# Kernel optimization log

Measured on AMD Instinct MI355X. Metric: run time of the kernel, lower is better.

Reference implementation:

```python
import jax, jax.numpy as jnp
import numpy as np

B, N, DIM = 4, 2048, 64  # batch, seq_len (== gate out dim), model dim (== dim_head)
H, DH = 8, 64            # heads, dim_head


def setup_inputs() -> dict:
    key = jax.random.key(0)
    ks = jax.random.split(key, 12)
    inner = H * DH
    inp = {
        'q': jax.random.normal(ks[0], (B, N, DIM), jnp.float32),
        'k': jax.random.normal(ks[1], (B, N, DIM), jnp.float32),
        'v': jax.random.normal(ks[2], (B, N, DIM), jnp.float32),
        'Wq': jax.random.normal(ks[3], (inner, DIM), jnp.float32) * 0.05,
        'Wk': jax.random.normal(ks[4], (inner, DIM), jnp.float32) * 0.05,
        'Wv': jax.random.normal(ks[5], (inner, DIM), jnp.float32) * 0.05,
        'Wo': jax.random.normal(ks[6], (DIM, inner), jnp.float32) * 0.05,
        'bo': jax.random.normal(ks[7], (DIM,), jnp.float32) * 0.05,
        'Wg': jax.random.normal(ks[8], (N, DIM), jnp.float32) * 0.05,
        's_local': jnp.float32(1.0),
        's_long': jnp.float32(1.0),
        # recurrent compressive-memory state; positive to avoid 0/0 of zero-init buffers
        'mem': jax.random.uniform(ks[9], (H, DH, DH), jnp.float32) + 0.5,
        'mem_norm': jax.random.uniform(ks[10], (H, N, 1), jnp.float32) + 0.5,
    }
    return inp


def _heads(x, W):
    # x: (B,N,DIM) @ W.T (DIM, H*DH) -> (B,H,N,DH)
    y = x @ W.T
    return y.reshape(x.shape[0], x.shape[1], H, DH).transpose(0, 2, 1, 3)


def reference(q, k, v, Wq, Wk, Wv, Wo, bo, Wg, s_local, s_long, mem, mem_norm):
    scale = DH ** -0.5
    qh, kh, vh = _heads(q, Wq), _heads(k, Wk), _heads(v, Wv)  # (B,H,N,DH)

    # local softmax attention, down-gated by (1 - sigmoid(local scalar))
    sim = jnp.einsum('bhnd,bhmd->bhnm', qh, kh) * scale
    local_attn = jax.nn.softmax(sim, axis=-1) * (1.0 - jax.nn.sigmoid(s_local))

    # query compressive memory: elu(q) @ M / (elu(q) * norm)
    eq = jax.nn.elu(qh)
    mem_q = jnp.einsum('bhnd,hde->bhne', eq, mem) / (eq * mem_norm[None])  # (B,H,N,DH)
    gated = jax.nn.sigmoid(s_long) * jnp.einsum('bhnd,md->bhnm', mem_q, Wg)  # (B,H,N,N)

    attn = local_attn + gated
    out = jnp.einsum('bhnm,bhmd->bhnd', attn, vh)
    out = out.transpose(0, 2, 1, 3).reshape(q.shape[0], q.shape[1], H * DH)
    out = out @ Wo.T + bo  # (B,N,DIM)

    # memory update (state side effect in the original forward)
    ek = jax.nn.elu(kh)
    v_term = vh - jnp.einsum('bhnd,hde->bhne', ek, mem) / (ek * mem_norm[None])
    new_mem = mem[None] + jnp.einsum('bhnd,bhne->bhde', ek, v_term)  # (B,H,DH,DH)
    new_norm = ek.sum(-1)  # (B,H,N)
    return out, new_mem, new_norm
```

## Files before the change

### kernel.cpp

```cpp
#include <hip/hip_runtime.h>
#include <math.h>


#define B_   4
#define N_   2048
#define H_   8
#define BH_  32
#define KP   72
#define SCLK 0.18033688f

typedef __bf16 bf16x8 __attribute__((ext_vector_type(8)));
typedef __bf16 bf16x4 __attribute__((ext_vector_type(4)));
typedef short  s16x4  __attribute__((ext_vector_type(4)));
typedef float  f32x4  __attribute__((ext_vector_type(4)));

__device__ __forceinline__ float eluf(float x) {
    return x > 0.0f ? x : expm1f(x);
}

__device__ __forceinline__ float fexp2(float x) {
    return __builtin_amdgcn_exp2f(x);
}

__device__ __forceinline__ f32x4 mfma16(bf16x4 a, bf16x4 b, f32x4 c) {
#if __has_builtin(__builtin_amdgcn_mfma_f32_16x16x16_bf16)
    return __builtin_amdgcn_mfma_f32_16x16x16_bf16(a, b, c, 0, 0, 0);
#else
    s16x4 ai, bi;
    __builtin_memcpy(&ai, &a, 8);
    __builtin_memcpy(&bi, &b, 8);
    return __builtin_amdgcn_mfma_f32_16x16x16bf16_1k(ai, bi, c, 0, 0, 0);
#endif
}

__global__ __launch_bounds__(256) void k_proj(
    const float* __restrict__ q, const float* __restrict__ k, const float* __restrict__ v,
    const float* __restrict__ Wq, const float* __restrict__ Wk, const float* __restrict__ Wv,
    __bf16* __restrict__ qb, float* __restrict__ kh, __bf16* __restrict__ kb,
    __bf16* __restrict__ vb, __bf16* __restrict__ vbT)
{
    const int which = blockIdx.z;
    const int h    = blockIdx.y;
    const int row0 = blockIdx.x * 64;
    const int tid  = threadIdx.x;
    const int b = row0 >> 11, nb = row0 & 2047;

    __shared__ __align__(16) float  AsT[64][68];
    __shared__ __align__(16) float  WsT[64][68];
    __shared__ __align__(16) __bf16 Cs[64 * 72];

    if (which == 2) {
        const int w = tid >> 6, lane = tid & 63;
        const int quad = lane >> 4, m = lane & 15;
        const float* ar = v + (size_t)(row0 + w * 16 + m) * 64;
        bf16x8 a0, a1;
        #pragma unroll
        for (int j = 0; j < 8; ++j) {
            a0[j] = (__bf16)ar[quad * 8 + j];
            a1[j] = (__bf16)ar[32 + quad * 8 + j];
        }
        f32x4 acc[4];
        #pragma unroll
        for (int t = 0; t < 4; ++t) {
            const float* wr = Wv + (size_t)(h * 64 + t * 16 + m) * 64;
            bf16x8 b0, b1;
            #pragma unroll
            for (int j = 0; j < 8; ++j) {
                b0[j] = (__bf16)wr[quad * 8 + j];
                b1[j] = (__bf16)wr[32 + quad * 8 + j];
            }
            f32x4 z = {0.f, 0.f, 0.f, 0.f};
            z = __builtin_amdgcn_mfma_f32_16x16x32_bf16(a0, b0, z, 0, 0, 0);
            acc[t] = __builtin_amdgcn_mfma_f32_16x16x32_bf16(a1, b1, z, 0, 0, 0);
        }
        #pragma unroll
        for (int t = 0; t < 4; ++t)
            #pragma unroll
            for (int r = 0; r < 4; ++r)
                Cs[(w * 16 + quad * 4 + r) * 72 + t * 16 + m] = (__bf16)acc[t][r];
        __syncthreads();
        const int rr = tid >> 2, csg = (tid & 3) * 16;
        bf16x8 r0 = *(const bf16x8*)&Cs[rr * 72 + csg];
        bf16x8 r1 = *(const bf16x8*)&Cs[rr * 72 + csg + 8];
        size_t gb = ((((size_t)b * H_ + h) * N_ + nb + rr) << 6) + csg;
        *(bf16x8*)&vb[gb]     = r0;
        *(bf16x8*)&vb[gb + 8] = r1;
        const int e = tid >> 2, ns = (tid & 3) * 16;
        bf16x8 t0, t1;
        #pragma unroll
        for (int j = 0; j < 8; ++j) {
            t0[j] = Cs[(ns + j) * 72 + e];
            t1[j] = Cs[(ns + 8 + j) * 72 + e];
        }
        size_t base = (((size_t)b * H_ + h) * 64 + e) * (size_t)N_ + nb + ns;
        *(bf16x8*)&vbT[base]     = t0;
        *(bf16x8*)&vbT[base + 8] = t1;
        return;
    }

    const float* __restrict__ src = (which == 0) ? q : k;
    const float* __restrict__ W   = (which == 0) ? Wq : Wk;
    for (int s = 0; s < 16; ++s) {
        int flat = s * 256 + tid;
        int r = flat >> 6, d = flat & 63;
        AsT[d][r] = src[(size_t)(row0 + r) * 64 + d];
        WsT[d][r] = W[(size_t)(h * 64 + r) * 64 + d];
    }
    __syncthreads();

    const int ty = tid >> 4, tx = tid & 15;
    float acc[4][4];
    #pragma unroll
    for (int i = 0; i < 4; ++i)
        #pragma unroll
        for (int j = 0; j < 4; ++j) acc[i][j] = 0.0f;
    for (int kd = 0; kd < 64; ++kd) {
        float4 a4 = *(const float4*)&AsT[kd][ty * 4];
        float4 w4 = *(const float4*)&WsT[kd][tx * 4];
        float a[4] = {a4.x, a4.y, a4.z, a4.w};
        float w[4] = {w4.x, w4.y, w4.z, w4.w};
        #pragma unroll
        for (int i = 0; i < 4; ++i)
            #pragma unroll
            for (int j = 0; j < 4; ++j) acc[i][j] = fmaf(a[i], w[j], acc[i][j]);
    }

    if (which == 0) {
        #pragma unroll
        for (int i = 0; i < 4; ++i) {
            size_t idx = ((((size_t)b * H_ + h) * N_ + nb + ty * 4 + i) << 6) + tx * 4;
            bf16x4 o4 = {(__bf16)acc[i][0], (__bf16)acc[i][1],
                         (__bf16)acc[i][2], (__bf16)acc[i][3]};
            *(bf16x4*)&qb[idx] = o4;
        }
    } else {
        #pragma unroll
        for (int i = 0; i < 4; ++i) {
            size_t idx = ((((size_t)b * H_ + h) * N_ + nb + ty * 4 + i) << 6) + tx * 4;
            *(float4*)&kh[idx] = make_float4(acc[i][0], acc[i][1], acc[i][2], acc[i][3]);
            bf16x4 o4 = {(__bf16)(acc[i][0] * SCLK), (__bf16)(acc[i][1] * SCLK),
                         (__bf16)(acc[i][2] * SCLK), (__bf16)(acc[i][3] * SCLK)};
            *(bf16x4*)&kb[idx] = o4;
        }
    }
}

__global__ __launch_bounds__(256) void k_memacc(
    const float* __restrict__ kh, const __bf16* __restrict__ vb,
    const float* __restrict__ mem, const float* __restrict__ mem_norm,
    float* __restrict__ pmem, float* __restrict__ out_norm)
{
    const int chunk = blockIdx.x;
    const int bh    = blockIdx.y;
    const int h     = bh & 7;
    const int n0    = chunk * 128;

    __shared__ __align__(16) __bf16 memT_hi[64 * KP], memT_lo[64 * KP];
    __shared__ __align__(16) __bf16 ekn_hi[64 * KP],  ekn_lo[64 * KP];
    __shared__ __align__(16) __bf16 ekT_hi[64 * KP],  ekT_lo[64 * KP];
    __shared__ __align__(16) __bf16 vtT_hi[64 * KP],  vtT_lo[64 * KP];

    const int tid  = threadIdx.x;
    const int w    = tid >> 6, lane = tid & 63;
    const int quad = lane >> 4, m = lane & 15;

    for (int s = 0; s < 16; ++s) {
        int flat = s * 256 + tid;
        int d = flat >> 6, e = flat & 63;
        float mv = mem[(size_t)h * 4096 + flat];
        __bf16 hi = (__bf16)mv;
        memT_hi[e * KP + d] = hi;
        memT_lo[e * KP + d] = (__bf16)(mv - (float)hi);
    }

    bf16x8 onesv;
    #pragma unroll
    for (int j = 0; j < 8; ++j) onesv[j] = (m == 0) ? (__bf16)1.0f : (__bf16)0.0f;

    f32x4 accM[4];
    #pragma unroll
    for (int t = 0; t < 4; ++t) { f32x4 z = {0.f, 0.f, 0.f, 0.f}; accM[t] = z; }
    __syncthreads();

    for (int sub = 0; sub < 2; ++sub) {
        const int nb = n0 + sub * 64;
        for (int rr = w; rr < 64; rr += 4) {
            const int n = nb + rr;
            float ekv = eluf(kh[((size_t)bh * N_ + n) * 64 + lane]);
            __bf16 hi = (__bf16)ekv;
            __bf16 lo = (__bf16)(ekv - (float)hi);
            ekn_hi[rr * KP + lane] = hi;
            ekn_lo[rr * KP + lane] = lo;
            ekT_hi[lane * KP + rr] = hi;
            ekT_lo[lane * KP + rr] = lo;
        }
        __syncthreads();

        f32x4 km[4];
        #pragma unroll
        for (int t = 0; t < 4; ++t) { f32x4 z = {0.f, 0.f, 0.f, 0.f}; km[t] = z; }
        f32x4 nsum = {0.f, 0.f, 0.f, 0.f};
        #pragma unroll
        for (int c2 = 0; c2 < 2; ++c2) {
            bf16x8 Ah = *(const bf16x8*)&ekn_hi[(w * 16 + m) * KP + c2 * 32 + quad * 8];
            bf16x8 Al = *(const bf16x8*)&ekn_lo[(w * 16 + m) * KP + c2 * 32 + quad * 8];
            nsum = __builtin_amdgcn_mfma_f32_16x16x32_bf16(Ah, onesv, nsum, 0, 0, 0);
            nsum = __builtin_amdgcn_mfma_f32_16x16x32_bf16(Al, onesv, nsum, 0, 0, 0);
            #pragma unroll
            for (int et = 0; et < 4; ++et) {
                bf16x8 Bh = *(const bf16x8*)&memT_hi[(et * 16 + m) * KP + c2 * 32 + quad * 8];
                bf16x8 Bl = *(const bf16x8*)&memT_lo[(et * 16 + m) * KP + c2 * 32 + quad * 8];
                km[et] = __builtin_amdgcn_mfma_f32_16x16x32_bf16(Al, Bh, km[et], 0, 0, 0);
                km[et] = __builtin_amdgcn_mfma_f32_16x16x32_bf16(Ah, Bl, km[et], 0, 0, 0);
                km[et] = __builtin_amdgcn_mfma_f32_16x16x32_bf16(Ah, Bh, km[et], 0, 0, 0);
            }
        }
        if (m == 0) {
            #pragma unroll
            for (int r = 0; r < 4; ++r)
                out_norm[(size_t)bh * N_ + nb + w * 16 + quad * 4 + r] = nsum[r];
        }
        float nrmv[4];
        #pragma unroll
        for (int r = 0; r < 4; ++r)
            nrmv[r] = mem_norm[(size_t)h * N_ + nb + w * 16 + quad * 4 + r];
        #pragma unroll
        for (int et = 0; et < 4; ++et) {
            #pragma unroll
            for (int r = 0; r < 4; ++r) {
                const int nl = w * 16 + quad * 4 + r;
                const int e  = et * 16 + m;
                float vh  = (float)vb[((size_t)bh * N_ + nb + nl) * 64 + e];
                float ekv = (float)ekn_hi[nl * KP + e] + (float)ekn_lo[nl * KP + e];
                float vt  = vh - km[et][r] * __builtin_amdgcn_rcpf(ekv * nrmv[r]);
                __bf16 hi = (__bf16)vt;
                vtT_hi[e * KP + nl] = hi;
                vtT_lo[e * KP + nl] = (__bf16)(vt - (float)hi);
            }
        }
        __syncthreads();

        #pragma unroll
        for (int c2 = 0; c2 < 2; ++c2) {
            bf16x8 Ah = *(const bf16x8*)&ekT_hi[(w * 16 + m) * KP + c2 * 32 + quad * 8];
            bf16x8 Al = *(const bf16x8*)&ekT_lo[(w * 16 + m) * KP + c2 * 32 + quad * 8];
            #pragma unroll
            for (int et = 0; et < 4; ++et) {
                bf16x8 Bh = *(const bf16x8*)&vtT_hi[(et * 16 + m) * KP + c2 * 32 + quad * 8];
                bf16x8 Bl = *(const bf16x8*)&vtT_lo[(et * 16 + m) * KP + c2 * 32 + quad * 8];
                accM[et] = __builtin_amdgcn_mfma_f32_16x16x32_bf16(Al, Bh, accM[et], 0, 0, 0);
                accM[et] = __builtin_amdgcn_mfma_f32_16x16x32_bf16(Ah, Bl, accM[et], 0, 0, 0);
                accM[et] = __builtin_amdgcn_mfma_f32_16x16x32_bf16(Ah, Bh, accM[et], 0, 0, 0);
            }
        }
        __syncthreads();
    }

    const size_t base = ((size_t)chunk * BH_ + bh) * 4096;
    #pragma unroll
    for (int et = 0; et < 4; ++et)
        #pragma unroll
        for (int r = 0; r < 4; ++r)
            pmem[base + (size_t)(w * 16 + quad * 4 + r) * 64 + et * 16 + m] =
                accM[et][r];
}

__global__ __launch_bounds__(256) void k_gv(
    const float* __restrict__ Wg, const __bf16* __restrict__ vbT,
    float* __restrict__ pGv)
{
    const int chunk = blockIdx.x;
    const int bh    = blockIdx.y;
    const int n0    = chunk * 128;
    __shared__ __align__(16) __bf16 WgT[64 * 136];
    const int tid  = threadIdx.x;
    const int w    = tid >> 6, lane = tid & 63;
    const int quad = lane >> 4, m = tid & 15;

    for (int s = 0; s < 8; ++s) {
        int f4 = s * 256 + tid;
        int n = f4 >> 4, dg = (f4 & 15) * 4;
        float4 wv = *(const float4*)&Wg[(size_t)(n0 + n) * 64 + dg];
        WgT[(dg + 0) * 136 + n] = (__bf16)wv.x;
        WgT[(dg + 1) * 136 + n] = (__bf16)wv.y;
        WgT[(dg + 2) * 136 + n] = (__bf16)wv.z;
        WgT[(dg + 3) * 136 + n] = (__bf16)wv.w;
    }
    __syncthreads();

    f32x4 acc[4];
    #pragma unroll
    for (int t = 0; t < 4; ++t) { f32x4 z = {0.f, 0.f, 0.f, 0.f}; acc[t] = z; }
    #pragma unroll
    for (int c = 0; c < 4; ++c) {
        bf16x8 Af = *(const bf16x8*)&WgT[(w * 16 + m) * 136 + c * 32 + quad * 8];
        #pragma unroll
        for (int et = 0; et < 4; ++et) {
            bf16x8 Bf = *(const bf16x8*)&vbT[((size_t)bh * 64 + et * 16 + m) * N_ +
                                             n0 + c * 32 + quad * 8];
            acc[et] = __builtin_amdgcn_mfma_f32_16x16x32_bf16(Af, Bf, acc[et], 0, 0, 0);
        }
    }
    const size_t base = ((size_t)chunk * BH_ + bh) * 4096;
    #pragma unroll
    for (int et = 0; et < 4; ++et)
        #pragma unroll
        for (int r = 0; r < 4; ++r)
            pGv[base + (size_t)(w * 16 + quad * 4 + r) * 64 + et * 16 + m] =
                acc[et][r];
}

__global__ __launch_bounds__(256) void k_reduce(
    const float* __restrict__ mem, const float* __restrict__ pmem,
    const float* __restrict__ pGv, float* __restrict__ out_mem, float* __restrict__ Gv)
{
    const int idx = blockIdx.x * 256 + threadIdx.x;
    const int bh = idx >> 12, h = bh & 7, de = idx & 4095;
    float sm = mem[(size_t)h * 4096 + de];
    float sg = 0.0f;
    #pragma unroll
    for (int c = 0; c < 16; ++c) {
        sm += pmem[(size_t)c * 131072 + idx];
        sg += pGv[(size_t)c * 131072 + idx];
    }
    out_mem[idx] = sm;
    Gv[idx] = sg;
}

__global__ __launch_bounds__(256, 4) void k_flash(
    const __bf16* __restrict__ qb, const __bf16* __restrict__ kb,
    const __bf16* __restrict__ vbT, const float* __restrict__ mem,
    const float* __restrict__ mem_norm, const float* __restrict__ Gv,
    const float* __restrict__ s_local_p, const float* __restrict__ s_long_p,
    __bf16* __restrict__ o)
{
    const int n0 = blockIdx.x * 128;
    const int bh = blockIdx.y;
    const int h  = bh & 7;
    const __bf16* __restrict__ kbp = kb  + (size_t)bh * N_ * 64;
    const __bf16* __restrict__ vtp = vbT + (size_t)bh * 64 * N_;

    __shared__ __align__(16) __bf16 Kb[64 * KP];
    __shared__ __align__(16) __bf16 VT[64 * KP];
    __shared__ __align__(16) __bf16 Pw[128 * KP];
    __shared__ float lsl[128];
    __shared__ float nrm_l[128];

    const int tid  = threadIdx.x;
    const int w    = tid >> 6, lane = tid & 63;
    const int quad = lane >> 4, m = lane & 15;
    const float gl   = 1.0f - 1.0f / (1.0f + __expf(-s_local_p[0]));
    const float sigg = 1.0f / (1.0f + __expf(-s_long_p[0]));

    if (tid < 128) nrm_l[tid] = mem_norm[(size_t)h * N_ + n0 + tid];

    const size_t q0 = ((size_t)bh * N_ + n0 + w * 32 + m) * 64;
    const size_t q1 = q0 + 16 * 64;
    bf16x8 qa00 = *(const bf16x8*)&qb[q0 + quad * 8];
    bf16x8 qa01 = *(const bf16x8*)&qb[q0 + 32 + quad * 8];
    bf16x8 qa10 = *(const bf16x8*)&qb[q1 + quad * 8];
    bf16x8 qa11 = *(const bf16x8*)&qb[q1 + 32 + quad * 8];

    f32x4 O0[4], O1[4];
    #pragma unroll
    for (int t = 0; t < 4; ++t) {
        f32x4 z = {0.f, 0.f, 0.f, 0.f};
        O0[t] = z; O1[t] = z;
    }
    float lsum0 = 0.f, lsum1 = 0.f;
    const int pr0 = w * 32, pr1 = w * 32 + 16;

    const int srow = tid >> 2, scg = (tid & 3) * 16;
    bf16x8 pk0 = *(const bf16x8*)&kbp[(size_t)srow * 64 + scg];
    bf16x8 pk1 = *(const bf16x8*)&kbp[(size_t)srow * 64 + scg + 8];
    bf16x8 pv0 = *(const bf16x8*)&vtp[(size_t)srow * N_ + scg];
    bf16x8 pv1 = *(const bf16x8*)&vtp[(size_t)srow * N_ + scg + 8];

    for (int c = 0; c < 32; ++c) {
        __syncthreads();
        *(bf16x8*)&Kb[srow * KP + scg]     = pk0;
        *(bf16x8*)&Kb[srow * KP + scg + 8] = pk1;
        *(bf16x8*)&VT[srow * KP + scg]     = pv0;
        *(bf16x8*)&VT[srow * KP + scg + 8] = pv1;
        __syncthreads();
        if (c + 1 < 32) {
            const size_t kn = (size_t)((c + 1) * 64 + srow) * 64 + scg;
            const size_t vn = (size_t)srow * N_ + (c + 1) * 64 + scg;
            pk0 = *(const bf16x8*)&kbp[kn];
            pk1 = *(const bf16x8*)&kbp[kn + 8];
            pv0 = *(const bf16x8*)&vtp[vn];
            pv1 = *(const bf16x8*)&vtp[vn + 8];
        }

        f32x4 s0[4], s1[4];
        #pragma unroll
        for (int t = 0; t < 4; ++t) {
            bf16x8 ka0 = *(const bf16x8*)&Kb[(t * 16 + m) * KP + quad * 8];
            bf16x8 ka1 = *(const bf16x8*)&Kb[(t * 16 + m) * KP + 32 + quad * 8];
            f32x4 z = {0.f, 0.f, 0.f, 0.f};
            z = __builtin_amdgcn_mfma_f32_16x16x32_bf16(ka0, qa00, z, 0, 0, 0);
            s0[t] = __builtin_amdgcn_mfma_f32_16x16x32_bf16(ka1, qa01, z, 0, 0, 0);
            f32x4 z2 = {0.f, 0.f, 0.f, 0.f};
            z2 = __builtin_amdgcn_mfma_f32_16x16x32_bf16(ka0, qa10, z2, 0, 0, 0);
            s1[t] = __builtin_amdgcn_mfma_f32_16x16x32_bf16(ka1, qa11, z2, 0, 0, 0);
        }

        bf16x4 pa0[4], pa1[4];
        #pragma unroll
        for (int t = 0; t < 4; ++t) {
            float p0 = fexp2(s0[t][0]), p1 = fexp2(s0[t][1]);
            float p2 = fexp2(s0[t][2]), p3 = fexp2(s0[t][3]);
            lsum0 += p0 + p1 + p2 + p3;
            bf16x4 pk = {(__bf16)p0, (__bf16)p1, (__bf16)p2, (__bf16)p3};
            pa0[t] = pk;
            float r0 = fexp2(s1[t][0]), r1 = fexp2(s1[t][1]);
            float r2 = fexp2(s1[t][2]), r3 = fexp2(s1[t][3]);
            lsum1 += r0 + r1 + r2 + r3;
            bf16x4 rk = {(__bf16)r0, (__bf16)r1, (__bf16)r2, (__bf16)r3};
            pa1[t] = rk;
        }

        #pragma unroll
        for (int t = 0; t < 4; ++t) {
            #pragma unroll
            for (int et = 0; et < 4; ++et) {
                bf16x4 vb4 = *(const bf16x4*)&VT[(et * 16 + m) * KP + t * 16 + quad * 4];
                O0[et] = mfma16(pa0[t], vb4, O0[et]);
                O1[et] = mfma16(pa1[t], vb4, O1[et]);
            }
        }
    }

    lsum0 += __shfl_xor(lsum0, 16, 64); lsum0 += __shfl_xor(lsum0, 32, 64);
    lsum1 += __shfl_xor(lsum1, 16, 64); lsum1 += __shfl_xor(lsum1, 32, 64);
    if (lane < 16) { lsl[pr0 + lane] = lsum0; lsl[pr1 + lane] = lsum1; }

    __syncthreads();
    for (int s2 = 0; s2 < 16; ++s2) {
        int flat = s2 * 256 + tid;
        int d = flat >> 6, e = flat & 63;
        Kb[e * KP + d] = (__bf16)mem[(size_t)h * 4096 + flat];
        VT[e * KP + d] = (__bf16)Gv[(size_t)bh * 4096 + flat];
    }
    __syncthreads();

    __bf16* op = o + ((size_t)bh * N_ + n0) * 64;
    #pragma unroll
    for (int s = 0; s < 2; ++s) {
        const int prs = w * 32 + s * 16;
        bf16x8 ea0, ea1;
        #pragma unroll
        for (int j = 0; j < 8; ++j) {
            ea0[j] = (__bf16)eluf((float)(s == 0 ? qa00[j] : qa10[j]));
            ea1[j] = (__bf16)eluf((float)(s == 0 ? qa01[j] : qa11[j]));
        }
        f32x4 num[4];
        #pragma unroll
        for (int t = 0; t < 4; ++t) {
            bf16x8 b0 = *(const bf16x8*)&Kb[(t * 16 + m) * KP + quad * 8];
            bf16x8 b1 = *(const bf16x8*)&Kb[(t * 16 + m) * KP + 32 + quad * 8];
            f32x4 z = {0.f, 0.f, 0.f, 0.f};
            z = __builtin_amdgcn_mfma_f32_16x16x32_bf16(ea0, b0, z, 0, 0, 0);
            num[t] = __builtin_amdgcn_mfma_f32_16x16x32_bf16(ea1, b1, z, 0, 0, 0);
        }
        *(bf16x8*)&Pw[(prs + m) * KP + quad * 8]      = ea0;
        *(bf16x8*)&Pw[(prs + m) * KP + 32 + quad * 8] = ea1;
        asm volatile("s_waitcnt lgkmcnt(0)" ::: "memory");
        float mq[4][4];
        #pragma unroll
        for (int t = 0; t < 4; ++t)
            #pragma unroll
            for (int r = 0; r < 4; ++r) {
                float eqv = (float)Pw[(prs + quad * 4 + r) * KP + t * 16 + m];
                mq[t][r] = num[t][r] / (eqv * nrm_l[prs + quad * 4 + r]);
            }
        #pragma unroll
        for (int t = 0; t < 4; ++t)
            #pragma unroll
            for (int r = 0; r < 4; ++r)
                Pw[(prs + quad * 4 + r) * KP + t * 16 + m] = (__bf16)mq[t][r];
        asm volatile("s_waitcnt lgkmcnt(0)" ::: "memory");
        bf16x8 ma0 = *(const bf16x8*)&Pw[(prs + m) * KP + quad * 8];
        bf16x8 ma1 = *(const bf16x8*)&Pw[(prs + m) * KP + 32 + quad * 8];

        #pragma unroll
        for (int t = 0; t < 4; ++t) {
            bf16x8 g0 = *(const bf16x8*)&VT[(t * 16 + m) * KP + quad * 8];
            bf16x8 g1 = *(const bf16x8*)&VT[(t * 16 + m) * KP + 32 + quad * 8];
            f32x4 z = {0.f, 0.f, 0.f, 0.f};
            z = __builtin_amdgcn_mfma_f32_16x16x32_bf16(ma0, g0, z, 0, 0, 0);
            f32x4 o2 = __builtin_amdgcn_mfma_f32_16x16x32_bf16(ma1, g1, z, 0, 0, 0);
            #pragma unroll
            for (int r = 0; r < 4; ++r) {
                const int qr = prs + quad * 4 + r;
                float val = ((s == 0) ? O0[t][r] : O1[t][r]) * (gl / lsl[qr])
                            + sigg * o2[r];
                op[(size_t)qr * 64 + t * 16 + m] = (__bf16)val;
            }
        }
    }
}

__global__ __launch_bounds__(256) void k_outproj(
    const __bf16* __restrict__ o, const float* __restrict__ Wo,
    const float* __restrict__ bo, float* __restrict__ out)
{
    const int row0 = blockIdx.x * 64;
    const int b = row0 >> 11, nb = row0 & 2047;
    __shared__ __align__(16) __bf16 WoS[64 * 40];
    const int tid  = threadIdx.x;
    const int w    = tid >> 6, lane = tid & 63;
    const int quad = lane >> 4, m = lane & 15;

    f32x4 acc[4];
    #pragma unroll
    for (int t = 0; t < 4; ++t) { f32x4 z = {0.f, 0.f, 0.f, 0.f}; acc[t] = z; }

    for (int kbk = 0; kbk < 16; ++kbk) {
        for (int s2 = 0; s2 < 8; ++s2) {
            int flat = s2 * 256 + tid;
            int n = flat >> 5, kk = flat & 31;
            WoS[n * 40 + kk] = (__bf16)Wo[(size_t)n * 512 + kbk * 32 + kk];
        }
        __syncthreads();
        const int hc = kbk >> 1;
        size_t arow = (((size_t)b * H_ + hc) * N_ + nb + w * 16 + m);
        bf16x8 af = *(const bf16x8*)&o[arow * 64 + (kbk & 1) * 32 + quad * 8];
        #pragma unroll
        for (int t = 0; t < 4; ++t) {
            bf16x8 bf_ = *(const bf16x8*)&WoS[(t * 16 + m) * 40 + quad * 8];
            acc[t] = __builtin_amdgcn_mfma_f32_16x16x32_bf16(af, bf_, acc[t], 0, 0, 0);
        }
        __syncthreads();
    }
    #pragma unroll
    for (int t = 0; t < 4; ++t) {
        float bias = bo[t * 16 + m];
        #pragma unroll
        for (int r = 0; r < 4; ++r)
            out[(size_t)(row0 + w * 16 + quad * 4 + r) * 64 + t * 16 + m] =
                acc[t][r] + bias;
    }
}

extern "C" void kernel_launch(void* const* d_in, const int* in_sizes, int n_in,
                              void* d_out, int out_size, void* d_ws, size_t ws_size,
                              hipStream_t stream)
{
    const float* q        = (const float*)d_in[0];
    const float* k        = (const float*)d_in[1];
    const float* v        = (const float*)d_in[2];
    const float* Wq       = (const float*)d_in[3];
    const float* Wk       = (const float*)d_in[4];
    const float* Wv       = (const float*)d_in[5];
    const float* Wo       = (const float*)d_in[6];
    const float* bo       = (const float*)d_in[7];
    const float* Wg       = (const float*)d_in[8];
    const float* s_local  = (const float*)d_in[9];
    const float* s_long   = (const float*)d_in[10];
    const float* mem      = (const float*)d_in[11];
    const float* mem_norm = (const float*)d_in[12];

    float* ws = (float*)d_ws;
    float*  kh  = ws;
    __bf16* qb  = (__bf16*)(ws + 4194304);
    __bf16* kb  = (__bf16*)(ws + 6291456);
    __bf16* vb  = (__bf16*)(ws + 8388608);
    __bf16* vbT = (__bf16*)(ws + 10485760);
    float*  Gv  = ws + 12582912;
    float*  pm  = ws + 12713984;
    float*  pg  = ws + 14811136;
    __bf16* o   = (__bf16*)(ws + 12713984);

    float* out      = (float*)d_out;
    float* out_mem  = out + 524288;
    float* out_norm = out + 655360;

    k_proj   <<<dim3(128, 8, 3), 256, 0, stream>>>(q, k, v, Wq, Wk, Wv,
                                                   qb, kh, kb, vb, vbT);
    k_memacc <<<dim3(16, 32),    256, 0, stream>>>(kh, vb, mem, mem_norm,
                                                   pm, out_norm);
    k_gv     <<<dim3(16, 32),    256, 0, stream>>>(Wg, vbT, pg);
    k_reduce <<<dim3(512),       256, 0, stream>>>(mem, pm, pg, out_mem, Gv);
    k_flash  <<<dim3(16, 32),    256, 0, stream>>>(qb, kb, vbT, mem, mem_norm, Gv,
                                                   s_local, s_long, o);
    k_outproj<<<dim3(128),       256, 0, stream>>>(o, Wo, bo, out);
}
```

Before: 202.9 us.

## Split flash KV loop across two 256-thread halves and merge partial outputs

```diff
diff --git a/kernel.cpp b/kernel.cpp
--- a/kernel.cpp
+++ b/kernel.cpp
@@ -327,7 +327,7 @@
     Gv[idx] = sg;
 }
 
-__global__ __launch_bounds__(256, 4) void k_flash(
+__global__ __launch_bounds__(512, 4) void k_flash(
     const __bf16* __restrict__ qb, const __bf16* __restrict__ kb,
     const __bf16* __restrict__ vbT, const float* __restrict__ mem,
     const float* __restrict__ mem_norm, const float* __restrict__ Gv,
@@ -340,21 +340,23 @@
     const __bf16* __restrict__ kbp = kb  + (size_t)bh * N_ * 64;
     const __bf16* __restrict__ vtp = vbT + (size_t)bh * 64 * N_;
 
-    __shared__ __align__(16) __bf16 Kb[64 * KP];
-    __shared__ __align__(16) __bf16 VT[64 * KP];
-    __shared__ __align__(16) __bf16 Pw[128 * KP];
-    __shared__ float lsl[128];
-    __shared__ float nrm_l[128];
+    __shared__ __align__(16) __bf16 Tiles[4 * 64 * KP];
+    __shared__ float lslA[128], lslB[128], nrm_l[128];
 
     const int tid  = threadIdx.x;
-    const int w    = tid >> 6, lane = tid & 63;
+    const int half = tid >> 8;
+    const int wl   = (tid >> 6) & 3;
+    const int lane = tid & 63;
     const int quad = lane >> 4, m = lane & 15;
     const float gl   = 1.0f - 1.0f / (1.0f + __expf(-s_local_p[0]));
     const float sigg = 1.0f / (1.0f + __expf(-s_long_p[0]));
 
+    __bf16* Kbuf = Tiles + (half * 2 + 0) * 64 * KP;
+    __bf16* Vbuf = Tiles + (half * 2 + 1) * 64 * KP;
+
     if (tid < 128) nrm_l[tid] = mem_norm[(size_t)h * N_ + n0 + tid];
 
-    const size_t q0 = ((size_t)bh * N_ + n0 + w * 32 + m) * 64;
+    const size_t q0 = ((size_t)bh * N_ + n0 + wl * 32 + m) * 64;
     const size_t q1 = q0 + 16 * 64;
     bf16x8 qa00 = *(const bf16x8*)&qb[q0 + quad * 8];
     bf16x8 qa01 = *(const bf16x8*)&qb[q0 + 32 + quad * 8];
@@ -368,24 +370,27 @@
         O0[t] = z; O1[t] = z;
     }
     float lsum0 = 0.f, lsum1 = 0.f;
-    const int pr0 = w * 32, pr1 = w * 32 + 16;
-
-    const int srow = tid >> 2, scg = (tid & 3) * 16;
-    bf16x8 pk0 = *(const bf16x8*)&kbp[(size_t)srow * 64 + scg];
-    bf16x8 pk1 = *(const bf16x8*)&kbp[(size_t)srow * 64 + scg + 8];
-    bf16x8 pv0 = *(const bf16x8*)&vtp[(size_t)srow * N_ + scg];
-    bf16x8 pv1 = *(const bf16x8*)&vtp[(size_t)srow * N_ + scg + 8];
-
-    for (int c = 0; c < 32; ++c) {
-        __syncthreads();
-        *(bf16x8*)&Kb[srow * KP + scg]     = pk0;
-        *(bf16x8*)&Kb[srow * KP + scg + 8] = pk1;
-        *(bf16x8*)&VT[srow * KP + scg]     = pv0;
-        *(bf16x8*)&VT[srow * KP + scg + 8] = pv1;
-        __syncthreads();
-        if (c + 1 < 32) {
-            const size_t kn = (size_t)((c + 1) * 64 + srow) * 64 + scg;
-            const size_t vn = (size_t)srow * N_ + (c + 1) * 64 + scg;
+    const int pr0 = wl * 32, pr1 = wl * 32 + 16;
+
+    const int ht = tid & 255;
+    const int srow = ht >> 2, scg = (ht & 3) * 16;
+    const int c0 = half * 16;
+    bf16x8 pk0 = *(const bf16x8*)&kbp[(size_t)(c0 * 64 + srow) * 64 + scg];
+    bf16x8 pk1 = *(const bf16x8*)&kbp[(size_t)(c0 * 64 + srow) * 64 + scg + 8];
+    bf16x8 pv0 = *(const bf16x8*)&vtp[(size_t)srow * N_ + c0 * 64 + scg];
+    bf16x8 pv1 = *(const bf16x8*)&vtp[(size_t)srow * N_ + c0 * 64 + scg + 8];
+
+    for (int cc = 0; cc < 16; ++cc) {
+        __syncthreads();
+        *(bf16x8*)&Kbuf[srow * KP + scg]     = pk0;
+        *(bf16x8*)&Kbuf[srow * KP + scg + 8] = pk1;
+        *(bf16x8*)&Vbuf[srow * KP + scg]     = pv0;
+        *(bf16x8*)&Vbuf[srow * KP + scg + 8] = pv1;
+        __syncthreads();
+        if (cc + 1 < 16) {
+            const int c = c0 + cc + 1;
+            const size_t kn = (size_t)(c * 64 + srow) * 64 + scg;
+            const size_t vn = (size_t)srow * N_ + c * 64 + scg;
             pk0 = *(const bf16x8*)&kbp[kn];
             pk1 = *(const bf16x8*)&kbp[kn + 8];
             pv0 = *(const bf16x8*)&vtp[vn];
@@ -395,8 +400,8 @@
         f32x4 s0[4], s1[4];
         #pragma unroll
         for (int t = 0; t < 4; ++t) {
-            bf16x8 ka0 = *(const bf16x8*)&Kb[(t * 16 + m) * KP + quad * 8];
-            bf16x8 ka1 = *(const bf16x8*)&Kb[(t * 16 + m) * KP + 32 + quad * 8];
+            bf16x8 ka0 = *(const bf16x8*)&Kbuf[(t * 16 + m) * KP + quad * 8];
+            bf16x8 ka1 = *(const bf16x8*)&Kbuf[(t * 16 + m) * KP + 32 + quad * 8];
             f32x4 z = {0.f, 0.f, 0.f, 0.f};
             z = __builtin_amdgcn_mfma_f32_16x16x32_bf16(ka0, qa00, z, 0, 0, 0);
             s0[t] = __builtin_amdgcn_mfma_f32_16x16x32_bf16(ka1, qa01, z, 0, 0, 0);
@@ -424,7 +429,7 @@
         for (int t = 0; t < 4; ++t) {
             #pragma unroll
             for (int et = 0; et < 4; ++et) {
-                bf16x4 vb4 = *(const bf16x4*)&VT[(et * 16 + m) * KP + t * 16 + quad * 4];
+                bf16x4 vb4 = *(const bf16x4*)&Vbuf[(et * 16 + m) * KP + t * 16 + quad * 4];
                 O0[et] = mfma16(pa0[t], vb4, O0[et]);
                 O1[et] = mfma16(pa1[t], vb4, O1[et]);
             }
@@ -433,70 +438,101 @@
 
     lsum0 += __shfl_xor(lsum0, 16, 64); lsum0 += __shfl_xor(lsum0, 32, 64);
     lsum1 += __shfl_xor(lsum1, 16, 64); lsum1 += __shfl_xor(lsum1, 32, 64);
-    if (lane < 16) { lsl[pr0 + lane] = lsum0; lsl[pr1 + lane] = lsum1; }
 
     __syncthreads();
-    for (int s2 = 0; s2 < 16; ++s2) {
-        int flat = s2 * 256 + tid;
+    __bf16* Ocomb = Tiles;
+    if (lane < 16) {
+        if (half == 0) { lslA[pr0 + lane] = lsum0; lslA[pr1 + lane] = lsum1; }
+        else           { lslB[pr0 + lane] = lsum0; lslB[pr1 + lane] = lsum1; }
+    }
+    if (half == 0) {
+        #pragma unroll
+        for (int t = 0; t < 4; ++t)
+            #pragma unroll
+            for (int r = 0; r < 4; ++r)
+                Ocomb[(size_t)(pr1 + quad * 4 + r) * 64 + t * 16 + m] = (__bf16)O1[t][r];
+    } else {
+        #pragma unroll
+        for (int t = 0; t < 4; ++t)
+            #pragma unroll
+            for (int r = 0; r < 4; ++r)
+                Ocomb[(size_t)(pr0 + quad * 4 + r) * 64 + t * 16 + m] = (__bf16)O0[t][r];
+    }
+    __syncthreads();
+    const int prs = (half == 0) ? pr0 : pr1;
+    f32x4 Om[4];
+    #pragma unroll
+    for (int t = 0; t < 4; ++t) {
+        f32x4 v = (half == 0) ? O0[t] : O1[t];
+        #pragma unroll
+        for (int r = 0; r < 4; ++r)
+            v[r] += (float)Ocomb[(size_t)(prs + quad * 4 + r) * 64 + t * 16 + m];
+        Om[t] = v;
+    }
+
+    __syncthreads();
+    __bf16* MT = Tiles + 2 * 64 * KP;
+    __bf16* GT = Tiles + 3 * 64 * KP;
+    for (int s2 = 0; s2 < 8; ++s2) {
+        int flat = s2 * 512 + tid;
         int d = flat >> 6, e = flat & 63;
-        Kb[e * KP + d] = (__bf16)mem[(size_t)h * 4096 + flat];
-        VT[e * KP + d] = (__bf16)Gv[(size_t)bh * 4096 + flat];
+        MT[e * KP + d] = (__bf16)mem[(size_t)h * 4096 + flat];
+        GT[e * KP + d] = (__bf16)Gv[(size_t)bh * 4096 + flat];
     }
     __syncthreads();
 
-    __bf16* op = o + ((size_t)bh * N_ + n0) * 64;
-    #pragma unroll
-    for (int s = 0; s < 2; ++s) {
-        const int prs = w * 32 + s * 16;
-        bf16x8 ea0, ea1;
-        #pragma unroll
-        for (int j = 0; j < 8; ++j) {
-            ea0[j] = (__bf16)eluf((float)(s == 0 ? qa00[j] : qa10[j]));
-            ea1[j] = (__bf16)eluf((float)(s == 0 ? qa01[j] : qa11[j]));
-        }
-        f32x4 num[4];
-        #pragma unroll
-        for (int t = 0; t < 4; ++t) {
-            bf16x8 b0 = *(const bf16x8*)&Kb[(t * 16 + m) * KP + quad * 8];
-            bf16x8 b1 = *(const bf16x8*)&Kb[(t * 16 + m) * KP + 32 + quad * 8];
-            f32x4 z = {0.f, 0.f, 0.f, 0.f};
-            z = __builtin_amdgcn_mfma_f32_16x16x32_bf16(ea0, b0, z, 0, 0, 0);
-            num[t] = __builtin_amdgcn_mfma_f32_16x16x32_bf16(ea1, b1, z, 0, 0, 0);
-        }
-        *(bf16x8*)&Pw[(prs + m) * KP + quad * 8]      = ea0;
-        *(bf16x8*)&Pw[(prs + m) * KP + 32 + quad * 8] = ea1;
-        asm volatile("s_waitcnt lgkmcnt(0)" ::: "memory");
-        float mq[4][4];
-        #pragma unroll
-        for (int t = 0; t < 4; ++t)
-            #pragma unroll
-            for (int r = 0; r < 4; ++r) {
-                float eqv = (float)Pw[(prs + quad * 4 + r) * KP + t * 16 + m];
-                mq[t][r] = num[t][r] / (eqv * nrm_l[prs + quad * 4 + r]);
-            }
-        #pragma unroll
-        for (int t = 0; t < 4; ++t)
-            #pragma unroll
-            for (int r = 0; r < 4; ++r)
-                Pw[(prs + quad * 4 + r) * KP + t * 16 + m] = (__bf16)mq[t][r];
-        asm volatile("s_waitcnt lgkmcnt(0)" ::: "memory");
-        bf16x8 ma0 = *(const bf16x8*)&Pw[(prs + m) * KP + quad * 8];
-        bf16x8 ma1 = *(const bf16x8*)&Pw[(prs + m) * KP + 32 + quad * 8];
-
-        #pragma unroll
-        for (int t = 0; t < 4; ++t) {
-            bf16x8 g0 = *(const bf16x8*)&VT[(t * 16 + m) * KP + quad * 8];
-            bf16x8 g1 = *(const bf16x8*)&VT[(t * 16 + m) * KP + 32 + quad * 8];
-            f32x4 z = {0.f, 0.f, 0.f, 0.f};
-            z = __builtin_amdgcn_mfma_f32_16x16x32_bf16(ma0, g0, z, 0, 0, 0);
-            f32x4 o2 = __builtin_amdgcn_mfma_f32_16x16x32_bf16(ma1, g1, z, 0, 0, 0);
-            #pragma unroll
-            for (int r = 0; r < 4; ++r) {
-                const int qr = prs + quad * 4 + r;
-                float val = ((s == 0) ? O0[t][r] : O1[t][r]) * (gl / lsl[qr])
-                            + sigg * o2[r];
-                op[(size_t)qr * 64 + t * 16 + m] = (__bf16)val;
-            }
+    __bf16* PwE = Tiles;
+    __bf16* op  = o + ((size_t)bh * N_ + n0) * 64;
+    bf16x8 qs0 = (half == 0) ? qa00 : qa10;
+    bf16x8 qs1 = (half == 0) ? qa01 : qa11;
+    bf16x8 ea0, ea1;
+    #pragma unroll
+    for (int j = 0; j < 8; ++j) {
+        ea0[j] = (__bf16)eluf((float)qs0[j]);
+        ea1[j] = (__bf16)eluf((float)qs1[j]);
+    }
+    f32x4 num[4];
+    #pragma unroll
+    for (int t = 0; t < 4; ++t) {
+        bf16x8 b0 = *(const bf16x8*)&MT[(t * 16 + m) * KP + quad * 8];
+        bf16x8 b1 = *(const bf16x8*)&MT[(t * 16 + m) * KP + 32 + quad * 8];
+        f32x4 z = {0.f, 0.f, 0.f, 0.f};
+        z = __builtin_amdgcn_mfma_f32_16x16x32_bf16(ea0, b0, z, 0, 0, 0);
+        num[t] = __builtin_amdgcn_mfma_f32_16x16x32_bf16(ea1, b1, z, 0, 0, 0);
+    }
+    *(bf16x8*)&PwE[(prs + m) * KP + quad * 8]      = ea0;
+    *(bf16x8*)&PwE[(prs + m) * KP + 32 + quad * 8] = ea1;
+    asm volatile("s_waitcnt lgkmcnt(0)" ::: "memory");
+    float mq[4][4];
+    #pragma unroll
+    for (int t = 0; t < 4; ++t)
+        #pragma unroll
+        for (int r = 0; r < 4; ++r) {
+            float eqv = (float)PwE[(prs + quad * 4 + r) * KP + t * 16 + m];
+            mq[t][r] = num[t][r] / (eqv * nrm_l[prs + quad * 4 + r]);
+        }
+    #pragma unroll
+    for (int t = 0; t < 4; ++t)
+        #pragma unroll
+        for (int r = 0; r < 4; ++r)
+            PwE[(prs + quad * 4 + r) * KP + t * 16 + m] = (__bf16)mq[t][r];
+    asm volatile("s_waitcnt lgkmcnt(0)" ::: "memory");
+    bf16x8 ma0 = *(const bf16x8*)&PwE[(prs + m) * KP + quad * 8];
+    bf16x8 ma1 = *(const bf16x8*)&PwE[(prs + m) * KP + 32 + quad * 8];
+
+    #pragma unroll
+    for (int t = 0; t < 4; ++t) {
+        bf16x8 g0 = *(const bf16x8*)&GT[(t * 16 + m) * KP + quad * 8];
+        bf16x8 g1 = *(const bf16x8*)&GT[(t * 16 + m) * KP + 32 + quad * 8];
+        f32x4 z = {0.f, 0.f, 0.f, 0.f};
+        z = __builtin_amdgcn_mfma_f32_16x16x32_bf16(ma0, g0, z, 0, 0, 0);
+        f32x4 o2 = __builtin_amdgcn_mfma_f32_16x16x32_bf16(ma1, g1, z, 0, 0, 0);
+        #pragma unroll
+        for (int r = 0; r < 4; ++r) {
+            const int qr = prs + quad * 4 + r;
+            float ls = lslA[qr] + lslB[qr];
+            float val = Om[t][r] * (gl / ls) + sigg * o2[r];
+            op[(size_t)qr * 64 + t * 16 + m] = (__bf16)val;
         }
     }
 }
@@ -582,7 +618,7 @@
                                                    pm, out_norm);
     k_gv     <<<dim3(16, 32),    256, 0, stream>>>(Wg, vbT, pg);
     k_reduce <<<dim3(512),       256, 0, stream>>>(mem, pm, pg, out_mem, Gv);
-    k_flash  <<<dim3(16, 32),    256, 0, stream>>>(qb, kb, vbT, mem, mem_norm, Gv,
+    k_flash  <<<dim3(16, 32),    512, 0, stream>>>(qb, kb, vbT, mem, mem_norm, Gv,
                                                    s_local, s_long, o);
     k_outproj<<<dim3(128),       256, 0, stream>>>(o, Wo, bo, out);
 }
```

New measurement: 336.3 us. 65.8% more time.
